# Performance work log

Hardware: AMD Instinct MI355X
Metric: run time of the kernel (lower is better)

Reference implementation:

```python
import jax, jax.numpy as jnp
import numpy as np

BETA = 0.5
ITERS = 20


def bjorck_orthonormalize(w, beta, iters):
    def body(w, _):
        wtw = jnp.matmul(w.T, w)            # [in, in]
        w = (1.0 + beta) * w - beta * jnp.matmul(w, wtw)
        return w, None
    w, _ = jax.lax.scan(body, w, None, length=iters)
    return w


def setup_inputs() -> dict:
    key = jax.random.key(0)
    k1, k2, k3 = jax.random.split(key, 3)
    x = jax.random.normal(k1, (4, 8192, 1024), dtype=jnp.float32)
    kernel = jax.random.normal(k2, (1024, 1024), dtype=jnp.float32)
    bias = jax.random.normal(k3, (1024,), dtype=jnp.float32)
    return {"x": x, "kernel": kernel, "bias": bias}


def reference(x, kernel, bias):
    # safe Bjorck scaling: sqrt(in_features * out_features)
    scaling = jnp.sqrt(jnp.asarray(kernel.shape[0] * kernel.shape[1], dtype=kernel.dtype))
    w = bjorck_orthonormalize(kernel / scaling, BETA, ITERS)  # [in, out]
    y = jnp.einsum('bsi,io->bso', x, w)
    y = y + bias.reshape((1, 1, -1))
    return y
```

## Files before the change

### kernel.cpp

```cpp
#include <hip/hip_runtime.h>
#include <cstdint>

typedef _Float16 half8 __attribute__((ext_vector_type(8)));
typedef _Float16 half4v __attribute__((ext_vector_type(4)));
typedef float f32x4 __attribute__((ext_vector_type(4)));

__device__ __forceinline__ void async_copy16(const void* g, void* l) {
    __builtin_amdgcn_global_load_lds((const __attribute__((address_space(1))) void*)g,
                                     (__attribute__((address_space(3))) void*)l, 16, 0, 0);
}

__global__ __launch_bounds__(256) void prep_w(const float* __restrict__ K,
                                              _Float16* __restrict__ w0,
                                              _Float16* __restrict__ w0T) {
    __shared__ float tile[64][65];
    const int t  = threadIdx.x;
    const int bi = blockIdx.y * 64;
    const int bj = blockIdx.x * 64;
    const int r0 = t >> 4;
    const int c4 = (t & 15) * 4;
#pragma unroll
    for (int rr = 0; rr < 4; ++rr) {
        int r = r0 + rr * 16;
        f32x4 v = *(const f32x4*)&K[(size_t)(bi + r) * 1024 + bj + c4];
        v *= 0.03125f;
        half4v h;
        h[0] = (_Float16)v[0]; h[1] = (_Float16)v[1];
        h[2] = (_Float16)v[2]; h[3] = (_Float16)v[3];
        *(half4v*)&w0[(size_t)(bi + r) * 1024 + bj + c4] = h;
        tile[r][c4 + 0] = v[0]; tile[r][c4 + 1] = v[1];
        tile[r][c4 + 2] = v[2]; tile[r][c4 + 3] = v[3];
    }
    __syncthreads();
    const int cT = t >> 4;
    const int rT = (t & 15) * 4;
#pragma unroll
    for (int cc = 0; cc < 4; ++cc) {
        int c = cT + cc * 16;
        half4v h;
        h[0] = (_Float16)tile[rT + 0][c]; h[1] = (_Float16)tile[rT + 1][c];
        h[2] = (_Float16)tile[rT + 2][c]; h[3] = (_Float16)tile[rT + 3][c];
        *(half4v*)&w0T[(size_t)(bj + c) * 1024 + bi + rT] = h;
    }
}

template <int EPI>
__global__ __launch_bounds__(512) void gemm1k(const _Float16* __restrict__ A,
                                              const _Float16* __restrict__ BT,
                                              const _Float16* __restrict__ wcur,
                                              _Float16* __restrict__ out,
                                              _Float16* __restrict__ outT) {
    __shared__ _Float16 sA[4][8192];
    __shared__ _Float16 sB[4][8192];
    const int t = threadIdx.x;
    const int b = blockIdx.x;
    const int xcd = b & 7, j = b >> 3;
    const int m0 = (((xcd & 1) << 3) + (j & 7)) << 6;
    const int n0 = (((xcd >> 1) << 2) + (j >> 3)) << 6;
    const int ln = t & 63, wv = t >> 6;
    const int wm = wv >> 1, wn = wv & 1;
    const int q  = ln >> 4, l15 = ln & 15;
    const int row0 = m0 + wm * 16 + q * 4;

    float wpre[2][4];
    if (EPI == 1) {
#pragma unroll
        for (int jn = 0; jn < 2; ++jn) {
            int col = n0 + wn * 32 + jn * 16 + l15;
#pragma unroll
            for (int r = 0; r < 4; ++r)
                wpre[jn][r] = (float)wcur[(size_t)(row0 + r) * 1024 + col];
        }
    }

    f32x4 acc[2];
#pragma unroll
    for (int jn = 0; jn < 2; ++jn) {
        acc[jn][0] = 0.f; acc[jn][1] = 0.f;
        acc[jn][2] = 0.f; acc[jn][3] = 0.f;
    }

    auto stage = [&](int buf, int k0) {
#pragma unroll
        for (int rnd = 0; rnd < 2; ++rnd) {
            int c = t + rnd * 512;
            int row = c >> 4, g = c & 15;
            int gs = g ^ (row & 15);
            async_copy16(A + (size_t)(m0 + row) * 1024 + k0 + gs * 8, &sA[buf][c * 8]);
            async_copy16(BT + (size_t)(n0 + row) * 1024 + k0 + gs * 8, &sB[buf][c * 8]);
        }
    };
    auto frag = [&](const _Float16* s, int row, int kc) -> half8 {
        return *(const half8*)&s[row * 128 + ((kc ^ (row & 15)) << 3)];
    };
    auto dostep = [&](int buf) {
#pragma unroll
        for (int kk = 0; kk < 4; ++kk) {
            half8 a0 = frag(sA[buf], wm * 16 + l15, kk * 4 + q);
            half8 b0 = frag(sB[buf], wn * 32 + 0  + l15, kk * 4 + q);
            half8 b1 = frag(sB[buf], wn * 32 + 16 + l15, kk * 4 + q);
            acc[0] = __builtin_amdgcn_mfma_f32_16x16x32_f16(a0, b0, acc[0], 0, 0, 0);
            acc[1] = __builtin_amdgcn_mfma_f32_16x16x32_f16(a0, b1, acc[1], 0, 0, 0);
        }
    };

    stage(0, 0);
    stage(1, 128);
    stage(2, 256);
#pragma unroll 1
    for (int it = 0; it < 6; ++it) {
        asm volatile("s_waitcnt vmcnt(8)\n\ts_barrier" ::: "memory");
        if (it < 5) stage((it + 3) & 3, (it + 3) * 128);
        dostep(it & 3);
    }
    asm volatile("s_waitcnt vmcnt(4)\n\ts_barrier" ::: "memory");
    dostep(2);
    asm volatile("s_waitcnt vmcnt(0)\n\ts_barrier" ::: "memory");
    dostep(3);

#pragma unroll
    for (int jn = 0; jn < 2; ++jn) {
        int col = n0 + wn * 32 + jn * 16 + l15;
        if (EPI == 0) {
#pragma unroll
            for (int r = 0; r < 4; ++r)
                out[(size_t)(row0 + r) * 1024 + col] = (_Float16)acc[jn][r];
        } else {
            half4v hT;
#pragma unroll
            for (int r = 0; r < 4; ++r) {
                float nv  = 1.5f * wpre[jn][r] - 4.8828125e-4f * acc[jn][r];
                _Float16 h = (_Float16)nv;
                out[(size_t)(row0 + r) * 1024 + col] = h;
                hT[r] = h;
            }
            *(half4v*)&outT[(size_t)col * 1024 + row0] = hT;
        }
    }
}

__global__ __launch_bounds__(256) void gemm_big(const float* __restrict__ X,
                                                const _Float16* __restrict__ BT,
                                                const float* __restrict__ bias,
                                                float* __restrict__ Y) {
    __shared__ _Float16 sA[2][128 * 40];
    __shared__ _Float16 sB[4][128 * 32];
    const int t   = threadIdx.x;
    const int bb  = blockIdx.x;
    const int xcd = bb & 7;
    const int jj  = bb >> 3;
    const int rr  = jj >> 5;
    const int ss  = jj & 31;
    const int mt  = rr * 32 + xcd * 4 + (ss >> 3);
    const int nt  = ss & 7;
    const int m0 = mt * 128, n0 = nt * 128;
    const int ln = t & 63, wv = t >> 6;
    const int wm = wv >> 1, wn = wv & 1;
    const int q  = ln >> 4, l15 = ln & 15;

    f32x4 acc[4][4];
#pragma unroll
    for (int i = 0; i < 4; ++i)
#pragma unroll
        for (int j = 0; j < 4; ++j) {
            acc[i][j][0] = 0.f; acc[i][j][1] = 0.f;
            acc[i][j][2] = 0.f; acc[i][j][3] = 0.f;
        }

    auto loadA = [&](int k0, f32x4* va) {
#pragma unroll
        for (int rnd = 0; rnd < 4; ++rnd) {
            int c = t + rnd * 256;
            int row = c >> 3, s4 = c & 7;
            va[rnd] = *(const f32x4*)&X[(size_t)(m0 + row) * 1024 + k0 + s4 * 4];
        }
    };
    auto writeA = [&](int buf, const f32x4* va) {
#pragma unroll
        for (int rnd = 0; rnd < 4; ++rnd) {
            int c = t + rnd * 256;
            int row = c >> 3, s4 = c & 7;
            half4v h;
            h[0] = (_Float16)va[rnd][0]; h[1] = (_Float16)va[rnd][1];
            h[2] = (_Float16)va[rnd][2]; h[3] = (_Float16)va[rnd][3];
            *(half4v*)&sA[buf][row * 40 + s4 * 4] = h;
        }
    };
    auto stageB = [&](int buf, int k0) {
#pragma unroll
        for (int rnd = 0; rnd < 2; ++rnd) {
            int c = t + rnd * 256;
            int row = c >> 2, s = c & 3;
            int gs = s ^ ((row >> 1) & 3);
            async_copy16(BT + (size_t)(n0 + row) * 1024 + k0 + gs * 8, &sB[buf][c * 8]);
        }
    };
    auto compute = [&](int t_) {
        half8 a[4], bfr[4];
#pragma unroll
        for (int im = 0; im < 4; ++im) {
            int row = wm * 64 + im * 16 + l15;
            a[im] = *(const half8*)&sA[t_ & 1][row * 40 + q * 8];
        }
#pragma unroll
        for (int jn = 0; jn < 4; ++jn) {
            int row = wn * 64 + jn * 16 + l15;
            bfr[jn] = *(const half8*)&sB[t_ & 3][row * 32 + ((q ^ ((row >> 1) & 3)) << 3)];
        }
#pragma unroll
        for (int im = 0; im < 4; ++im)
#pragma unroll
            for (int jn = 0; jn < 4; ++jn)
                acc[im][jn] = __builtin_amdgcn_mfma_f32_16x16x32_f16(a[im], bfr[jn], acc[im][jn], 0, 0, 0);
    };

    f32x4 vaA[4], vaB[4];
    loadA(0, vaA);
    stageB(0, 0);
    writeA(0, vaA);
    loadA(32, vaB);
    stageB(1, 32);
    stageB(2, 64);

#define BODY(T, VLD, VWR, CNT)                                                \
    {                                                                         \
        asm volatile("s_waitcnt vmcnt(" #CNT ") lgkmcnt(0)\n\ts_barrier" ::: "memory"); \
        if ((T) + 2 < 32) loadA(((T) + 2) * 32, VLD);                         \
        if ((T) + 3 < 32) stageB(((T) + 3) & 3, ((T) + 3) * 32);              \
        compute(T);                                                           \
        writeA(((T) + 1) & 1, VWR);                                           \
    }

#pragma unroll 1
    for (int tp = 0; tp < 15; ++tp) {
        int te = tp * 2;
        BODY(te, vaA, vaB, 8);
        BODY(te + 1, vaB, vaA, 8);
    }
    BODY(30, vaA, vaB, 6);
#undef BODY
    asm volatile("s_waitcnt vmcnt(0) lgkmcnt(0)\n\ts_barrier" ::: "memory");
    compute(31);

#pragma unroll
    for (int jn = 0; jn < 4; ++jn) {
        int col = n0 + wn * 64 + jn * 16 + l15;
        float bv = bias[col];
#pragma unroll
        for (int im = 0; im < 4; ++im) {
            int row0 = m0 + wm * 64 + im * 16 + q * 4;
#pragma unroll
            for (int r = 0; r < 4; ++r)
                Y[(size_t)(row0 + r) * 1024 + col] = acc[im][jn][r] * 0.03125f + bv;
        }
    }
}

extern "C" void kernel_launch(void* const* d_in, const int* in_sizes, int n_in,
                              void* d_out, int out_size, void* d_ws, size_t ws_size,
                              hipStream_t stream) {
    (void)in_sizes; (void)n_in; (void)out_size; (void)ws_size;
    const float* x    = (const float*)d_in[0];
    const float* kern = (const float*)d_in[1];
    const float* bias = (const float*)d_in[2];
    float* y = (float*)d_out;

    char* ws = (char*)d_ws;
    const size_t SZ = (size_t)1024 * 1024 * sizeof(_Float16);
    _Float16* wh[2] = {(_Float16*)(ws + 0 * SZ), (_Float16*)(ws + 1 * SZ)};
    _Float16* wT[2] = {(_Float16*)(ws + 2 * SZ), (_Float16*)(ws + 3 * SZ)};
    _Float16* Sh    = (_Float16*)(ws + 4 * SZ);

    prep_w<<<dim3(16, 16), 256, 0, stream>>>(kern, wh[0], wT[0]);

    for (int it = 0; it < 20; ++it) {
        int c = it & 1, n = c ^ 1;
        gemm1k<0><<<256, 512, 0, stream>>>(wT[c], wT[c], nullptr, Sh, nullptr);
        gemm1k<1><<<256, 512, 0, stream>>>(wh[c], Sh, wh[c], wh[n], wT[n]);
    }
    gemm_big<<<2048, 256, 0, stream>>>(x, wT[0], bias, y);
}
```

Baseline: 725.3 us.

## Enlarge final GEMM tile to 256x256 with 512 threads and BK=64

The final x·W GEMM moves from 128x128 tiles with 256 threads and 32-wide K steps to 256x256 tiles with 512 threads (8 waves, each computing 128x64) and 64-wide K steps. It also switches from a 4-deep to a 2-deep B buffer with XOR-swizzled 64-wide LDS rows for both A and B. The aim is more data reuse per LDS byte and fewer global loads per FLOP. In exchange it uses more registers per thread (128 accumulators plus 8 prefetch vectors) and 128KB of LDS, launches only 512 blocks, and has a shallower pipeline.

```diff
diff --git a/kernel.cpp b/kernel.cpp
--- a/kernel.cpp
+++ b/kernel.cpp
@@ -139,116 +139,126 @@
     }
 }
 
-__global__ __launch_bounds__(256) void gemm_big(const float* __restrict__ X,
+__global__ __launch_bounds__(512) void gemm_big(const float* __restrict__ X,
                                                 const _Float16* __restrict__ BT,
                                                 const float* __restrict__ bias,
                                                 float* __restrict__ Y) {
-    __shared__ _Float16 sA[2][128 * 40];
-    __shared__ _Float16 sB[4][128 * 32];
-    const int t   = threadIdx.x;
-    const int bb  = blockIdx.x;
-    const int xcd = bb & 7;
-    const int jj  = bb >> 3;
-    const int rr  = jj >> 5;
-    const int ss  = jj & 31;
-    const int mt  = rr * 32 + xcd * 4 + (ss >> 3);
-    const int nt  = ss & 7;
-    const int m0 = mt * 128, n0 = nt * 128;
+    __shared__ _Float16 sA[2][256 * 64];
+    __shared__ _Float16 sB[2][256 * 64];
+    const int t    = threadIdx.x;
+    const int b    = blockIdx.x;
+    const int xcd  = b & 7;
+    const int j    = b >> 3;
+    const int rnd_ = j >> 5;
+    const int jj   = j & 31;
+    const int mt   = rnd_ * 64 + xcd * 8 + (jj >> 2);
+    const int nt   = jj & 3;
+    const int m0 = mt * 256, n0 = nt * 256;
     const int ln = t & 63, wv = t >> 6;
-    const int wm = wv >> 1, wn = wv & 1;
+    const int wm = wv >> 2, wn = wv & 3;
     const int q  = ln >> 4, l15 = ln & 15;
 
-    f32x4 acc[4][4];
-#pragma unroll
-    for (int i = 0; i < 4; ++i)
-#pragma unroll
-        for (int j = 0; j < 4; ++j) {
-            acc[i][j][0] = 0.f; acc[i][j][1] = 0.f;
-            acc[i][j][2] = 0.f; acc[i][j][3] = 0.f;
-        }
-
-    auto loadA = [&](int k0, f32x4* va) {
+    f32x4 acc[8][4];
+#pragma unroll
+    for (int i = 0; i < 8; ++i)
+#pragma unroll
+        for (int jn = 0; jn < 4; ++jn) {
+            acc[i][jn][0] = 0.f; acc[i][jn][1] = 0.f;
+            acc[i][jn][2] = 0.f; acc[i][jn][3] = 0.f;
+        }
+
+    auto loadX = [&](int k0, f32x4* va) {
 #pragma unroll
         for (int rnd = 0; rnd < 4; ++rnd) {
-            int c = t + rnd * 256;
-            int row = c >> 3, s4 = c & 7;
-            va[rnd] = *(const f32x4*)&X[(size_t)(m0 + row) * 1024 + k0 + s4 * 4];
+            int c = t + rnd * 512;
+            int row = c >> 3, g = c & 7;
+            const float* p = &X[(size_t)(m0 + row) * 1024 + k0 + g * 8];
+            va[rnd * 2 + 0] = *(const f32x4*)p;
+            va[rnd * 2 + 1] = *(const f32x4*)(p + 4);
         }
     };
     auto writeA = [&](int buf, const f32x4* va) {
 #pragma unroll
         for (int rnd = 0; rnd < 4; ++rnd) {
-            int c = t + rnd * 256;
-            int row = c >> 3, s4 = c & 7;
-            half4v h;
-            h[0] = (_Float16)va[rnd][0]; h[1] = (_Float16)va[rnd][1];
-            h[2] = (_Float16)va[rnd][2]; h[3] = (_Float16)va[rnd][3];
-            *(half4v*)&sA[buf][row * 40 + s4 * 4] = h;
+            int c = t + rnd * 512;
+            int row = c >> 3, g = c & 7;
+            half8 h;
+#pragma unroll
+            for (int i = 0; i < 4; ++i) {
+                h[i]     = (_Float16)va[rnd * 2 + 0][i];
+                h[4 + i] = (_Float16)va[rnd * 2 + 1][i];
+            }
+            *(half8*)&sA[buf][row * 64 + ((g ^ (row & 7)) << 3)] = h;
         }
     };
     auto stageB = [&](int buf, int k0) {
 #pragma unroll
-        for (int rnd = 0; rnd < 2; ++rnd) {
-            int c = t + rnd * 256;
-            int row = c >> 2, s = c & 3;
-            int gs = s ^ ((row >> 1) & 3);
-            async_copy16(BT + (size_t)(n0 + row) * 1024 + k0 + gs * 8, &sB[buf][c * 8]);
-        }
-    };
-    auto compute = [&](int t_) {
-        half8 a[4], bfr[4];
-#pragma unroll
-        for (int im = 0; im < 4; ++im) {
-            int row = wm * 64 + im * 16 + l15;
-            a[im] = *(const half8*)&sA[t_ & 1][row * 40 + q * 8];
-        }
-#pragma unroll
-        for (int jn = 0; jn < 4; ++jn) {
-            int row = wn * 64 + jn * 16 + l15;
-            bfr[jn] = *(const half8*)&sB[t_ & 3][row * 32 + ((q ^ ((row >> 1) & 3)) << 3)];
-        }
-#pragma unroll
-        for (int im = 0; im < 4; ++im)
-#pragma unroll
-            for (int jn = 0; jn < 4; ++jn)
-                acc[im][jn] = __builtin_amdgcn_mfma_f32_16x16x32_f16(a[im], bfr[jn], acc[im][jn], 0, 0, 0);
-    };
-
-    f32x4 vaA[4], vaB[4];
-    loadA(0, vaA);
+        for (int rnd = 0; rnd < 4; ++rnd) {
+            int c = t + rnd * 512;
+            int row = c >> 3, g = c & 7;
+            int gs = g ^ (row & 7);
+            async_copy16(BT + (size_t)(n0 + row) * 1024 + k0 + gs * 8,
+                         &sB[buf][c * 8]);
+        }
+    };
+    auto compute = [&](int tb) {
+        const _Float16* A_ = sA[tb & 1];
+        const _Float16* B_ = sB[tb & 1];
+#pragma unroll
+        for (int kk = 0; kk < 2; ++kk) {
+            const int gidx = kk * 4 + q;
+            half8 a[8], bf[4];
+#pragma unroll
+            for (int im = 0; im < 8; ++im) {
+                int row = wm * 128 + im * 16 + l15;
+                a[im] = *(const half8*)&A_[row * 64 + ((gidx ^ (row & 7)) << 3)];
+            }
+#pragma unroll
+            for (int jn = 0; jn < 4; ++jn) {
+                int row = wn * 64 + jn * 16 + l15;
+                bf[jn] = *(const half8*)&B_[row * 64 + ((gidx ^ (row & 7)) << 3)];
+            }
+#pragma unroll
+            for (int im = 0; im < 8; ++im)
+#pragma unroll
+                for (int jn = 0; jn < 4; ++jn)
+                    acc[im][jn] = __builtin_amdgcn_mfma_f32_16x16x32_f16(
+                        a[im], bf[jn], acc[im][jn], 0, 0, 0);
+        }
+    };
+
+    f32x4 vaA[8], vaB[8];
+    loadX(0, vaA);
     stageB(0, 0);
     writeA(0, vaA);
-    loadA(32, vaB);
-    stageB(1, 32);
-    stageB(2, 64);
+    loadX(64, vaB);
 
 #define BODY(T, VLD, VWR, CNT)                                                \
     {                                                                         \
         asm volatile("s_waitcnt vmcnt(" #CNT ") lgkmcnt(0)\n\ts_barrier" ::: "memory"); \
-        if ((T) + 2 < 32) loadA(((T) + 2) * 32, VLD);                         \
-        if ((T) + 3 < 32) stageB(((T) + 3) & 3, ((T) + 3) * 32);              \
+        if ((T) + 1 < 16) stageB(((T) + 1) & 1, ((T) + 1) * 64);              \
+        if ((T) + 2 < 16) loadX(((T) + 2) * 64, VLD);                         \
+        if ((T) + 1 < 16) writeA(((T) + 1) & 1, VWR);                         \
         compute(T);                                                           \
-        writeA(((T) + 1) & 1, VWR);                                           \
     }
 
 #pragma unroll 1
-    for (int tp = 0; tp < 15; ++tp) {
+    for (int tp = 0; tp < 7; ++tp) {
         int te = tp * 2;
         BODY(te, vaA, vaB, 8);
         BODY(te + 1, vaB, vaA, 8);
     }
-    BODY(30, vaA, vaB, 6);
+    BODY(14, vaA, vaB, 8);
+    BODY(15, vaB, vaA, 0);
 #undef BODY
-    asm volatile("s_waitcnt vmcnt(0) lgkmcnt(0)\n\ts_barrier" ::: "memory");
-    compute(31);
 
 #pragma unroll
     for (int jn = 0; jn < 4; ++jn) {
         int col = n0 + wn * 64 + jn * 16 + l15;
         float bv = bias[col];
 #pragma unroll
-        for (int im = 0; im < 4; ++im) {
-            int row0 = m0 + wm * 64 + im * 16 + q * 4;
+        for (int im = 0; im < 8; ++im) {
+            int row0 = m0 + wm * 128 + im * 16 + q * 4;
 #pragma unroll
             for (int r = 0; r < 4; ++r)
                 Y[(size_t)(row0 + r) * 1024 + col] = acc[im][jn][r] * 0.03125f + bv;
@@ -278,5 +288,5 @@
         gemm1k<0><<<256, 512, 0, stream>>>(wT[c], wT[c], nullptr, Sh, nullptr);
         gemm1k<1><<<256, 512, 0, stream>>>(wh[c], Sh, wh[c], wh[n], wT[n]);
     }
-    gemm_big<<<2048, 256, 0, stream>>>(x, wT[0], bias, y);
-}
+    gemm_big<<<512, 512, 0, stream>>>(x, wT[0], bias, y);
+}
```

Measured after the change: 676.3 us. 6.8% less time.
